# Performance work log

Measured on AMD Instinct MI355X. Metric: run time of the kernel, lower is better.

## Reference

```python
import jax, jax.numpy as jnp
import numpy as np

B, T, C = 1, 2048, 1024
H, D = 16, 64  # n_head, head_size (n_query_groups == n_head -> plain MHA)


def build_rope_cache(seq_len, n_elem, base=10000):
    theta = 1.0 / (base ** (jnp.arange(0, n_elem, 2, dtype=jnp.float32) / n_elem))
    idx_theta = jnp.outer(jnp.arange(seq_len, dtype=jnp.float32), theta)
    idx_theta = jnp.concatenate([idx_theta, idx_theta], axis=-1)  # torch .repeat(1, 2)
    return jnp.cos(idx_theta), jnp.sin(idx_theta)


def apply_rope(x, cos, sin):
    d = x.shape[-1]
    x1, x2 = x[..., : d // 2], x[..., d // 2 :]
    rotated = jnp.concatenate([-x2, x1], axis=-1)
    return x * cos + rotated * sin


def fastmax_attention(q, k, v):
    """Fastmax: first-order Taylor approx of softmax attention, causal, O(n*d^2).
    score(i,j) = 1 + q_i . k_j (temperature=1, zero RPE, no dropout);
    out_i = sum_{j<=i} score*v_j / sum_{j<=i} score, via causal cumulative sums."""
    n = q.shape[2]
    kcum = jnp.cumsum(k, axis=2)                                       # (B,H,T,D)
    kvcum = jnp.cumsum(jnp.einsum('bhnd,bhne->bhnde', k, v), axis=2)   # (B,H,T,D,D)
    den = jnp.arange(1, n + 1, dtype=q.dtype) + jnp.einsum('bhnd,bhnd->bhn', q, kcum)
    num = jnp.cumsum(v, axis=2) + jnp.einsum('bhnd,bhnde->bhne', q, kvcum)
    return num / den[..., None]


def setup_inputs() -> dict:
    key = jax.random.key(0)
    k1, k2, k3 = jax.random.split(key, 3)
    scale = 0.02
    x = jax.random.normal(k1, (B, T, C), dtype=jnp.float32)
    w_attn = jax.random.normal(k2, (3 * H * D, C), dtype=jnp.float32) * scale
    w_proj = jax.random.normal(k3, (C, H * D), dtype=jnp.float32) * scale
    cos, sin = build_rope_cache(T, D)
    return {"x": x, "w_attn": w_attn, "w_proj": w_proj, "cos": cos, "sin": sin}


def reference(x, w_attn, w_proj, cos, sin):
    Bx, Tx, Cx = x.shape
    qkv = x @ w_attn.T                                  # (B,T,3HD)
    qkv = qkv.reshape(Bx, Tx, H, 3, D).transpose(0, 2, 3, 1, 4)  # (B,H,3,T,D)
    q, k, v = qkv[:, :, 0], qkv[:, :, 1], qkv[:, :, 2]
    q = apply_rope(q, cos, sin)
    k = apply_rope(k, cos, sin)
    y = fastmax_attention(q, k, v)                      # (B,H,T,D)
    y = y.transpose(0, 2, 1, 3).reshape(Bx, Tx, H * D)
    return y @ w_proj.T
```

## Files before the change

### kernel.cpp

```cpp
#include <hip/hip_runtime.h>

#define T_LEN 2048
#define C_DIM 1024
#define H_NUM 16
#define D_DIM 64
#define QKV_N (3 * H_NUM * D_DIM)
#define L_CHK 64
#define NC (T_LEN / L_CHK)

typedef _Float16 h8 __attribute__((ext_vector_type(8)));
typedef _Float16 h4 __attribute__((ext_vector_type(4)));
typedef float f32x4 __attribute__((ext_vector_type(4)));

__global__ __launch_bounds__(256) void split3_f16(
    const float* __restrict__ x, _Float16* __restrict__ xh,
    _Float16* __restrict__ xl, const float* __restrict__ wa,
    _Float16* __restrict__ wah, _Float16* __restrict__ wal,
    const float* __restrict__ wp, _Float16* __restrict__ wph) {
  int i = (blockIdx.x * 256 + threadIdx.x) * 8;
  const float* src;
  _Float16 *dh, *dl = nullptr;
  int base;
  if (i < 2097152) {
    src = x; dh = xh; dl = xl; base = i;
  } else if (i < 2097152 + 3145728) {
    src = wa; dh = wah; dl = wal; base = i - 2097152;
  } else {
    src = wp; dh = wph; base = i - 5242880;
  }
  float4 a = *(const float4*)(src + base);
  float4 b = *(const float4*)(src + base + 4);
  float v[8] = {a.x, a.y, a.z, a.w, b.x, b.y, b.z, b.w};
  h8 hv, lv;
#pragma unroll
  for (int j = 0; j < 8; ++j) {
    float s = v[j] * 64.f;
    _Float16 h = (_Float16)s;
    hv[j] = h;
    lv[j] = (_Float16)(s - (float)h);
  }
  *(h8*)(dh + base) = hv;
  if (dl) *(h8*)(dl + base) = lv;
}

template <int BN, bool ROPE, bool SPLIT3>
__global__ __launch_bounds__(256) void gemm_nt_f16(
    const _Float16* __restrict__ Ah, const _Float16* __restrict__ Al,
    const _Float16* __restrict__ Bh, const _Float16* __restrict__ Bl,
    float* __restrict__ C, const float* __restrict__ cosb,
    const float* __restrict__ sinb, float* __restrict__ qout,
    float* __restrict__ kout, float* __restrict__ vout, int M, int N, int K,
    float outscale) {
  constexpr int NJ = BN / 32;
  constexpr int NARR = SPLIT3 ? 2 : 1;
  constexpr int GEMM_BYTES = (64 * 64 * 2 + BN * 64 * 2) * NARR;
  constexpr int ROPE_BYTES = ROPE ? (2 * 64 * 64 * 4) : 0;
  constexpr int SMEM_BYTES = GEMM_BYTES > ROPE_BYTES ? GEMM_BYTES : ROPE_BYTES;
  __shared__ __align__(16) char smem[SMEM_BYTES];
  _Float16* sAh = (_Float16*)smem;
  _Float16* sAl = sAh + 64 * 64;
  _Float16* sBh = sAh + 64 * 64 * NARR;
  _Float16* sBl = sBh + BN * 64;
  const int tid = threadIdx.x;
  const int wave = tid >> 6;
  const int lane = tid & 63;
  const int bm = blockIdx.y * 64;
  const int bn = blockIdx.x * BN;
  const int wm = wave >> 1;
  const int wn = wave & 1;
  const int srow = lane >> 3;
  const int sblk = ((lane & 7) ^ srow) * 8;
  const int quad = lane >> 4;
  const int lrow = lane & 15;

  f32x4 acc[2][NJ];
#pragma unroll
  for (int i = 0; i < 2; ++i)
#pragma unroll
    for (int j = 0; j < NJ; ++j) acc[i][j] = (f32x4){0.f, 0.f, 0.f, 0.f};

  for (int k0 = 0; k0 < K; k0 += 64) {
#pragma unroll
    for (int it = 0; it < 2; ++it) {
      const int ch = wave + it * 4;
      const int row = ch * 8 + srow;
      const _Float16* ga = Ah + (size_t)(bm + row) * K + k0 + sblk;
      __builtin_amdgcn_global_load_lds(
          (const __attribute__((address_space(1))) void*)ga,
          (__attribute__((address_space(3))) void*)(sAh + ch * 512), 16, 0, 0);
      if constexpr (SPLIT3) {
        const _Float16* gb = Al + (size_t)(bm + row) * K + k0 + sblk;
        __builtin_amdgcn_global_load_lds(
            (const __attribute__((address_space(1))) void*)gb,
            (__attribute__((address_space(3))) void*)(sAl + ch * 512), 16, 0,
            0);
      }
    }
#pragma unroll
    for (int it = 0; it < BN / 32; ++it) {
      const int ch = wave + it * 4;
      const int row = ch * 8 + srow;
      const _Float16* ga = Bh + (size_t)(bn + row) * K + k0 + sblk;
      __builtin_amdgcn_global_load_lds(
          (const __attribute__((address_space(1))) void*)ga,
          (__attribute__((address_space(3))) void*)(sBh + ch * 512), 16, 0, 0);
      if constexpr (SPLIT3) {
        const _Float16* gb = Bl + (size_t)(bn + row) * K + k0 + sblk;
        __builtin_amdgcn_global_load_lds(
            (const __attribute__((address_space(1))) void*)gb,
            (__attribute__((address_space(3))) void*)(sBl + ch * 512), 16, 0,
            0);
      }
    }
    __syncthreads();
#pragma unroll
    for (int kk = 0; kk < 2; ++kk) {
      h8 ah[2], al[2], bh[NJ], bl[NJ];
#pragma unroll
      for (int i = 0; i < 2; ++i) {
        const int row = wm * 32 + i * 16 + lrow;
        const int ra = row * 64 + (((kk * 4 + quad) ^ (row & 7)) * 8);
        ah[i] = *(const h8*)&sAh[ra];
        if constexpr (SPLIT3) al[i] = *(const h8*)&sAl[ra];
      }
#pragma unroll
      for (int j = 0; j < NJ; ++j) {
        const int row = wn * (BN / 2) + j * 16 + lrow;
        const int rb = row * 64 + (((kk * 4 + quad) ^ (row & 7)) * 8);
        bh[j] = *(const h8*)&sBh[rb];
        if constexpr (SPLIT3) bl[j] = *(const h8*)&sBl[rb];
      }
#pragma unroll
      for (int i = 0; i < 2; ++i)
#pragma unroll
        for (int j = 0; j < NJ; ++j) {
          acc[i][j] = __builtin_amdgcn_mfma_f32_16x16x32_f16(
              ah[i], bh[j], acc[i][j], 0, 0, 0);
          if constexpr (SPLIT3) {
            acc[i][j] = __builtin_amdgcn_mfma_f32_16x16x32_f16(
                ah[i], bl[j], acc[i][j], 0, 0, 0);
            acc[i][j] = __builtin_amdgcn_mfma_f32_16x16x32_f16(
                al[i], bh[j], acc[i][j], 0, 0, 0);
          }
        }
    }
    __syncthreads();
  }
  if constexpr (!ROPE) {
#pragma unroll
    for (int i = 0; i < 2; ++i) {
      const int rbase = bm + wm * 32 + i * 16 + quad * 4;
#pragma unroll
      for (int j = 0; j < NJ; ++j) {
        const int col = bn + wn * (BN / 2) + j * 16 + lrow;
#pragma unroll
        for (int r = 0; r < 4; ++r)
          C[(size_t)(rbase + r) * N + col] = acc[i][j][r] * outscale;
      }
    }
  } else {
    float* cs = (float*)smem;
    float* sn = cs + 4096;
#pragma unroll
    for (int m = 0; m < 4; ++m) {
      int el = (tid + m * 256) * 4;
      *(float4*)&cs[el] = *(const float4*)&cosb[bm * D_DIM + el];
      *(float4*)&sn[el] = *(const float4*)&sinb[bm * D_DIM + el];
    }
    __syncthreads();
    const int colbase = bn + wn * 64;
    const int type = (colbase >> 6) % 3;
    const int head = colbase / 192;
    float* dst = (type == 0) ? qout : (type == 1) ? kout : vout;
    const size_t hbase = (size_t)head * T_LEN * D_DIM;
#pragma unroll
    for (int i = 0; i < 2; ++i) {
      const int tloc0 = wm * 32 + i * 16 + quad * 4;
#pragma unroll
      for (int r = 0; r < 4; ++r) {
        const int tloc = tloc0 + r;
        float* trow = dst + hbase + (size_t)(bm + tloc) * D_DIM;
#pragma unroll
        for (int j = 0; j < NJ; ++j) {
          const int d = j * 16 + lrow;
          float val = acc[i][j][r] * outscale;
          if (type < 2) {
            float rotv = ((j < 2) ? -acc[i][j + 2][r] : acc[i][j - 2][r]) *
                         outscale;
            val = val * cs[tloc * D_DIM + d] + rotv * sn[tloc * D_DIM + d];
          }
          trow[d] = val;
        }
      }
    }
  }
}

__global__ __launch_bounds__(256) void chunk_kv(
    const float* __restrict__ k, const float* __restrict__ v,
    float* __restrict__ kvchunk, float* __restrict__ kschunk,
    float* __restrict__ vschunk) {
  __shared__ float Ks[L_CHK][D_DIM];
  __shared__ float Vs[L_CHK][D_DIM];
  int blk = blockIdx.x;
  const size_t off = ((size_t)(blk / NC) * T_LEN + (blk % NC) * L_CHK) * D_DIM;
  int tid = threadIdx.x;
#pragma unroll
  for (int m = 0; m < 4; ++m) {
    int el = (tid + m * 256) * 4;
    *(float4*)&((float*)Ks)[el] = *(const float4*)&k[off + el];
    *(float4*)&((float*)Vs)[el] = *(const float4*)&v[off + el];
  }
  __syncthreads();
  int e = tid & 63;
  int q2 = tid >> 6;
  float acc[16] = {};
  for (int t = 0; t < L_CHK; ++t) {
    float ve = Vs[t][e];
#pragma unroll
    for (int m = 0; m < 16; ++m) acc[m] += Ks[t][q2 * 16 + m] * ve;
  }
  float* outb = kvchunk + (size_t)blk * (D_DIM * D_DIM);
#pragma unroll
  for (int m = 0; m < 16; ++m) outb[(q2 * 16 + m) * D_DIM + e] = acc[m];
  if (tid < 64) {
    float s = 0.f;
    for (int t = 0; t < L_CHK; ++t) s += Ks[t][tid];
    kschunk[(size_t)blk * D_DIM + tid] = s;
  } else if (tid < 128) {
    float s = 0.f;
    for (int t = 0; t < L_CHK; ++t) s += Vs[t][tid - 64];
    vschunk[(size_t)blk * D_DIM + (tid - 64)] = s;
  }
}

__global__ __launch_bounds__(256) void scan_fused(
    const float* __restrict__ kvchunk, float* __restrict__ kvpref,
    const float* __restrict__ kschunk, const float* __restrict__ vschunk,
    float* __restrict__ kspref, float* __restrict__ vspref) {
  int b = blockIdx.x;
  int tid = threadIdx.x;
  if (b < 256) {
    int gid = b * 256 + tid;
    int h = gid >> 12;
    int de = gid & 4095;
    float vals[NC];
#pragma unroll
    for (int c = 0; c < NC; ++c)
      vals[c] = kvchunk[((size_t)(h * NC + c) << 12) + de];
    float run = 0.f;
#pragma unroll
    for (int c = 0; c < NC; ++c) {
      kvpref[((size_t)(h * NC + c) << 12) + de] = run;
      run += vals[c];
    }
  } else {
    int gid = (b - 256) * 256 + tid;
    int h = gid >> 6, d = gid & 63;
    float kv_[NC], vv_[NC];
#pragma unroll
    for (int c = 0; c < NC; ++c) {
      size_t idx = (size_t)(h * NC + c) * 64 + d;
      kv_[c] = kschunk[idx];
      vv_[c] = vschunk[idx];
    }
    float rk = 0.f, rv = 0.f;
#pragma unroll
    for (int c = 0; c < NC; ++c) {
      size_t idx = (size_t)(h * NC + c) * 64 + d;
      kspref[idx] = rk;
      vspref[idx] = rv;
      rk += kv_[c];
      rv += vv_[c];
    }
  }
}

__global__ __launch_bounds__(256) void attn_out(
    const float* __restrict__ q, const float* __restrict__ k,
    const float* __restrict__ v, const float* __restrict__ kvpref,
    const float* __restrict__ kspref, const float* __restrict__ vspref,
    _Float16* __restrict__ yh) {
  __shared__ float Ks[L_CHK * D_DIM];
  __shared__ float Vs[L_CHK * D_DIM];
  __shared__ float Ss[L_CHK][L_CHK + 1];
  int blk = blockIdx.x;
  int h = blk / NC, c = blk % NC;
  int tid = threadIdx.x;
  int r = tid & 63;
  int g = tid >> 6;
  const size_t off = ((size_t)h * T_LEN + c * L_CHK) * D_DIM;
#pragma unroll
  for (int m = 0; m < 4; ++m) {
    int el = (tid + m * 256) * 4;
    *(float4*)&Ks[el] = *(const float4*)&k[off + el];
    *(float4*)&Vs[el] = *(const float4*)&v[off + el];
  }
  float qv[D_DIM];
#pragma unroll
  for (int i = 0; i < 16; ++i) {
    float4 t4 = *(const float4*)&q[off + r * D_DIM + i * 4];
    qv[i * 4 + 0] = t4.x; qv[i * 4 + 1] = t4.y;
    qv[i * 4 + 2] = t4.z; qv[i * 4 + 3] = t4.w;
  }
  __syncthreads();
#pragma unroll
  for (int jj = 0; jj < 16; ++jj) {
    int j = g * 16 + jj;
    const float4* krow = (const float4*)&Ks[j * D_DIM];
    float sdot = 0.f;
#pragma unroll
    for (int i = 0; i < 16; ++i) {
      float4 kj = krow[i];
      sdot += qv[i * 4] * kj.x + qv[i * 4 + 1] * kj.y + qv[i * 4 + 2] * kj.z +
              qv[i * 4 + 3] * kj.w;
    }
    Ss[r][j] = (j <= r) ? (sdot + 1.f) : 0.f;
  }
  __syncthreads();
  const float* kvp = kvpref + (size_t)blk * (D_DIM * D_DIM);
#pragma unroll
  for (int m = 0; m < 4; ++m) {
    int el = (tid + m * 256) * 4;
    *(float4*)&Ks[el] = *(const float4*)&kvp[el];
  }
  __syncthreads();
  const float* ksp = kspref + (size_t)blk * D_DIM;
  const float* vsp = vspref + (size_t)blk * D_DIM;
  float den = (float)(c * L_CHK);
#pragma unroll
  for (int i = 0; i < 16; ++i) {
    float4 kk = *(const float4*)&ksp[i * 4];
    den += qv[i * 4] * kk.x + qv[i * 4 + 1] * kk.y + qv[i * 4 + 2] * kk.z +
           qv[i * 4 + 3] * kk.w;
  }
  float4 num[4];
#pragma unroll
  for (int i = 0; i < 4; ++i) num[i] = *(const float4*)&vsp[g * 16 + i * 4];
#pragma unroll
  for (int d = 0; d < D_DIM; ++d) {
    float qd = qv[d];
    const float4* kvrow = (const float4*)&Ks[d * D_DIM + g * 16];
#pragma unroll
    for (int i = 0; i < 4; ++i) {
      float4 k4 = kvrow[i];
      num[i].x += qd * k4.x; num[i].y += qd * k4.y;
      num[i].z += qd * k4.z; num[i].w += qd * k4.w;
    }
  }
  float rs = 0.f;
#pragma unroll 8
  for (int j = 0; j < L_CHK; ++j) {
    float f = Ss[r][j];
    rs += f;
    const float4* vrow = (const float4*)&Vs[j * D_DIM + g * 16];
#pragma unroll
    for (int i = 0; i < 4; ++i) {
      float4 v4 = vrow[i];
      num[i].x += f * v4.x; num[i].y += f * v4.y;
      num[i].z += f * v4.z; num[i].w += f * v4.w;
    }
  }
  den += rs;
  float inv = 1.f / den;
  int t = c * L_CHK + r;
  size_t ybase = (size_t)t * (H_NUM * D_DIM) + h * D_DIM + g * 16;
#pragma unroll
  for (int i = 0; i < 4; ++i) {
    h4 hv;
    hv[0] = (_Float16)(num[i].x * inv);
    hv[1] = (_Float16)(num[i].y * inv);
    hv[2] = (_Float16)(num[i].z * inv);
    hv[3] = (_Float16)(num[i].w * inv);
    *(h4*)&yh[ybase + i * 4] = hv;
  }
}

extern "C" void kernel_launch(void* const* d_in, const int* in_sizes, int n_in,
                              void* d_out, int out_size, void* d_ws,
                              size_t ws_size, hipStream_t stream) {
  const float* x = (const float*)d_in[0];
  const float* w_attn = (const float*)d_in[1];
  const float* w_proj = (const float*)d_in[2];
  const float* cosb = (const float*)d_in[3];
  const float* sinb = (const float*)d_in[4];
  float* out = (float*)d_out;

  char* ws = (char*)d_ws;
  float* kvchunk = (float*)ws;
  float* kvpref = (float*)(ws + 8388608);
  float* qbuf = (float*)(ws + 25165824);
  float* kbuf = (float*)(ws + 25165824 + 8388608);
  float* vbuf = (float*)(ws + 25165824 + 16777216);
  _Float16* xh = (_Float16*)(ws + 50331648);
  _Float16* xl = (_Float16*)(ws + 50331648 + 4194304);
  _Float16* yh = (_Float16*)(ws + 50331648);
  _Float16* wah = (_Float16*)(ws + 58720256);
  _Float16* wal = (_Float16*)(ws + 58720256 + 6291456);
  float* kschunk = (float*)(ws + 58720256);
  float* vschunk = (float*)(ws + 58720256 + 131072);
  float* kspref = (float*)(ws + 58720256 + 262144);
  float* vspref = (float*)(ws + 58720256 + 393216);
  _Float16* wph = (_Float16*)(ws + 71303168);

  split3_f16<<<3072, 256, 0, stream>>>(x, xh, xl, w_attn, wah, wal, w_proj,
                                       wph);

  {
    dim3 grid(QKV_N / 128, T_LEN / 64);
    gemm_nt_f16<128, true, true><<<grid, 256, 0, stream>>>(
        xh, xl, wah, wal, nullptr, cosb, sinb, qbuf, kbuf, vbuf, T_LEN, QKV_N,
        C_DIM, 1.f / 4096.f);
  }
  chunk_kv<<<H_NUM * NC, 256, 0, stream>>>(kbuf, vbuf, kvchunk, kschunk,
                                           vschunk);
  scan_fused<<<260, 256, 0, stream>>>(kvchunk, kvpref, kschunk, vschunk,
                                      kspref, vspref);
  attn_out<<<H_NUM * NC, 256, 0, stream>>>(qbuf, kbuf, vbuf, kvpref, kspref,
                                           vspref, yh);
  {
    dim3 grid(C_DIM / 64, T_LEN / 64);
    gemm_nt_f16<64, false, false><<<grid, 256, 0, stream>>>(
        yh, nullptr, wph, nullptr, out, nullptr, nullptr, nullptr, nullptr,
        nullptr, T_LEN, C_DIM, C_DIM, 1.f / 64.f);
  }
}
```

Before: 173.7 us.

## Move intra-chunk attention and chunk KV sums onto split-f16 MFMA

The QKV GEMM epilogue now writes q and k as hi/lo f16 pairs and also emits transposed k and v (via an LDS bounce) in hi/lo f16. The chunk KV outer-product kernel and the attention-output kernel are rewritten to use 16x16x32 f16 MFMA with three-term split products, including the score matrix, row sums and prefix-state contributions. This is meant to replace scalar FP32 FMA loops with matrix-core work and halve the bytes read per element. In exchange it adds extra epilogue writes and barriers in the GEMM and some precision loss from the split-f16 approximation.

```diff
diff --git a/kernel.cpp b/kernel.cpp
--- a/kernel.cpp
+++ b/kernel.cpp
@@ -43,18 +43,30 @@
   if (dl) *(h8*)(dl + base) = lv;
 }
 
+__device__ __forceinline__ void split8(float4 a, float4 b, h8& hi, h8& lo) {
+  float v[8] = {a.x, a.y, a.z, a.w, b.x, b.y, b.z, b.w};
+#pragma unroll
+  for (int m = 0; m < 8; ++m) {
+    _Float16 hh = (_Float16)v[m];
+    hi[m] = hh;
+    lo[m] = (_Float16)(v[m] - (float)hh);
+  }
+}
+
 template <int BN, bool ROPE, bool SPLIT3>
 __global__ __launch_bounds__(256) void gemm_nt_f16(
     const _Float16* __restrict__ Ah, const _Float16* __restrict__ Al,
     const _Float16* __restrict__ Bh, const _Float16* __restrict__ Bl,
     float* __restrict__ C, const float* __restrict__ cosb,
-    const float* __restrict__ sinb, float* __restrict__ qout,
-    float* __restrict__ kout, float* __restrict__ vout, int M, int N, int K,
-    float outscale) {
+    const float* __restrict__ sinb, _Float16* __restrict__ qh_,
+    _Float16* __restrict__ ql_, _Float16* __restrict__ kh_,
+    _Float16* __restrict__ kl_, _Float16* __restrict__ kTh_,
+    _Float16* __restrict__ kTl_, _Float16* __restrict__ vTh_,
+    _Float16* __restrict__ vTl_, int M, int N, int K, float outscale) {
   constexpr int NJ = BN / 32;
   constexpr int NARR = SPLIT3 ? 2 : 1;
   constexpr int GEMM_BYTES = (64 * 64 * 2 + BN * 64 * 2) * NARR;
-  constexpr int ROPE_BYTES = ROPE ? (2 * 64 * 64 * 4) : 0;
+  constexpr int ROPE_BYTES = ROPE ? (2 * 64 * 64 * 4 + 64 * 64 * 4) : 0;
   constexpr int SMEM_BYTES = GEMM_BYTES > ROPE_BYTES ? GEMM_BYTES : ROPE_BYTES;
   __shared__ __align__(16) char smem[SMEM_BYTES];
   _Float16* sAh = (_Float16*)smem;
@@ -161,6 +173,7 @@
   } else {
     float* cs = (float*)smem;
     float* sn = cs + 4096;
+    float* bounce = sn + 4096;
 #pragma unroll
     for (int m = 0; m < 4; ++m) {
       int el = (tid + m * 256) * 4;
@@ -171,66 +184,160 @@
     const int colbase = bn + wn * 64;
     const int type = (colbase >> 6) % 3;
     const int head = colbase / 192;
-    float* dst = (type == 0) ? qout : (type == 1) ? kout : vout;
-    const size_t hbase = (size_t)head * T_LEN * D_DIM;
-#pragma unroll
-    for (int i = 0; i < 2; ++i) {
-      const int tloc0 = wm * 32 + i * 16 + quad * 4;
+    const size_t hb = (size_t)head * T_LEN * D_DIM;
+    float fv[2][4][4];
+#pragma unroll
+    for (int i = 0; i < 2; ++i)
 #pragma unroll
       for (int r = 0; r < 4; ++r) {
-        const int tloc = tloc0 + r;
-        float* trow = dst + hbase + (size_t)(bm + tloc) * D_DIM;
-#pragma unroll
-        for (int j = 0; j < NJ; ++j) {
+        const int tloc = wm * 32 + i * 16 + quad * 4 + r;
+#pragma unroll
+        for (int j = 0; j < 4; ++j) {
           const int d = j * 16 + lrow;
           float val = acc[i][j][r] * outscale;
           if (type < 2) {
-            float rotv = ((j < 2) ? -acc[i][j + 2][r] : acc[i][j - 2][r]) *
-                         outscale;
+            float rotv =
+                ((j < 2) ? -acc[i][j + 2][r] : acc[i][j - 2][r]) * outscale;
             val = val * cs[tloc * D_DIM + d] + rotv * sn[tloc * D_DIM + d];
           }
-          trow[d] = val;
+          fv[i][r][j] = val;
         }
       }
-    }
-  }
-}
-
-__global__ __launch_bounds__(256) void chunk_kv(
-    const float* __restrict__ k, const float* __restrict__ v,
+    if (type < 2) {
+      _Float16* dh = (type == 0 ? qh_ : kh_) + hb;
+      _Float16* dl = (type == 0 ? ql_ : kl_) + hb;
+#pragma unroll
+      for (int i = 0; i < 2; ++i)
+#pragma unroll
+        for (int r = 0; r < 4; ++r) {
+          const size_t trow =
+              (size_t)(bm + wm * 32 + i * 16 + quad * 4 + r) * D_DIM;
+#pragma unroll
+          for (int j = 0; j < 4; ++j) {
+            const int d = j * 16 + lrow;
+            float f = fv[i][r][j];
+            _Float16 hh = (_Float16)f;
+            dh[trow + d] = hh;
+            dl[trow + d] = (_Float16)(f - (float)hh);
+          }
+        }
+    }
+    const bool doT = (type >= 1);
+    _Float16* th = (type == 1 ? kTh_ : vTh_) + hb;
+    _Float16* tl = (type == 1 ? kTl_ : vTl_) + hb;
+#pragma unroll
+    for (int half = 0; half < 2; ++half) {
+      __syncthreads();
+      if (wn == half && doT) {
+#pragma unroll
+        for (int i = 0; i < 2; ++i)
+#pragma unroll
+          for (int r = 0; r < 4; ++r) {
+            const int tloc = wm * 32 + i * 16 + quad * 4 + r;
+#pragma unroll
+            for (int j = 0; j < 4; ++j) {
+              const int d = j * 16 + lrow;
+              bounce[tloc * 64 + (d ^ tloc)] = fv[i][r][j];
+            }
+          }
+      }
+      __syncthreads();
+      if (wn == half && doT) {
+        const int lt = wm * 64 + lane;
+        const int e = lt >> 1;
+        const int tg0 = (lt & 1) * 32;
+#pragma unroll
+        for (int s8 = 0; s8 < 4; ++s8) {
+          h8 hv, lv;
+#pragma unroll
+          for (int s = 0; s < 8; ++s) {
+            const int t = tg0 + s8 * 8 + s;
+            float f = bounce[t * 64 + (e ^ t)];
+            _Float16 hh = (_Float16)f;
+            hv[s] = hh;
+            lv[s] = (_Float16)(f - (float)hh);
+          }
+          *(h8*)&th[(size_t)e * T_LEN + bm + tg0 + s8 * 8] = hv;
+          *(h8*)&tl[(size_t)e * T_LEN + bm + tg0 + s8 * 8] = lv;
+        }
+      }
+    }
+  }
+}
+
+__global__ __launch_bounds__(256) void chunk_kvT(
+    const _Float16* __restrict__ kTh, const _Float16* __restrict__ kTl,
+    const _Float16* __restrict__ vTh, const _Float16* __restrict__ vTl,
     float* __restrict__ kvchunk, float* __restrict__ kschunk,
     float* __restrict__ vschunk) {
-  __shared__ float Ks[L_CHK][D_DIM];
-  __shared__ float Vs[L_CHK][D_DIM];
-  int blk = blockIdx.x;
-  const size_t off = ((size_t)(blk / NC) * T_LEN + (blk % NC) * L_CHK) * D_DIM;
-  int tid = threadIdx.x;
-#pragma unroll
-  for (int m = 0; m < 4; ++m) {
-    int el = (tid + m * 256) * 4;
-    *(float4*)&((float*)Ks)[el] = *(const float4*)&k[off + el];
-    *(float4*)&((float*)Vs)[el] = *(const float4*)&v[off + el];
-  }
-  __syncthreads();
-  int e = tid & 63;
-  int q2 = tid >> 6;
-  float acc[16] = {};
-  for (int t = 0; t < L_CHK; ++t) {
-    float ve = Vs[t][e];
-#pragma unroll
-    for (int m = 0; m < 16; ++m) acc[m] += Ks[t][q2 * 16 + m] * ve;
-  }
-  float* outb = kvchunk + (size_t)blk * (D_DIM * D_DIM);
-#pragma unroll
-  for (int m = 0; m < 16; ++m) outb[(q2 * 16 + m) * D_DIM + e] = acc[m];
+  const int blk = blockIdx.x;
+  const int h = blk / NC, c = blk % NC;
+  const int tid = threadIdx.x;
+  const int wave = tid >> 6, lane = tid & 63;
+  const int quad = lane >> 4, lrow = lane & 15;
+  const size_t hb = (size_t)h * D_DIM * T_LEN;
+  const int tb = c * L_CHK;
+  h8 avh[2], avl[2];
+  {
+    const _Float16* pa = vTh + hb + (size_t)(wave * 16 + lrow) * T_LEN + tb +
+                         quad * 8;
+    const _Float16* pal = vTl + hb + (size_t)(wave * 16 + lrow) * T_LEN + tb +
+                          quad * 8;
+    avh[0] = *(const h8*)pa;
+    avh[1] = *(const h8*)(pa + 32);
+    avl[0] = *(const h8*)pal;
+    avl[1] = *(const h8*)(pal + 32);
+  }
+  f32x4 accv[4];
+#pragma unroll
+  for (int dt = 0; dt < 4; ++dt) accv[dt] = (f32x4){0.f, 0.f, 0.f, 0.f};
+#pragma unroll
+  for (int dt = 0; dt < 4; ++dt) {
+    const _Float16* pb = kTh + hb + (size_t)(dt * 16 + lrow) * T_LEN + tb +
+                         quad * 8;
+    const _Float16* pbl = kTl + hb + (size_t)(dt * 16 + lrow) * T_LEN + tb +
+                          quad * 8;
+#pragma unroll
+    for (int ks = 0; ks < 2; ++ks) {
+      h8 bh = *(const h8*)(pb + ks * 32);
+      h8 bl = *(const h8*)(pbl + ks * 32);
+      accv[dt] = __builtin_amdgcn_mfma_f32_16x16x32_f16(avh[ks], bh, accv[dt],
+                                                        0, 0, 0);
+      accv[dt] = __builtin_amdgcn_mfma_f32_16x16x32_f16(avh[ks], bl, accv[dt],
+                                                        0, 0, 0);
+      accv[dt] = __builtin_amdgcn_mfma_f32_16x16x32_f16(avl[ks], bh, accv[dt],
+                                                        0, 0, 0);
+    }
+  }
+  float* ob = kvchunk + (size_t)blk * (D_DIM * D_DIM);
+#pragma unroll
+  for (int dt = 0; dt < 4; ++dt)
+#pragma unroll
+    for (int r = 0; r < 4; ++r)
+      ob[(wave * 16 + quad * 4 + r) * D_DIM + dt * 16 + lrow] = accv[dt][r];
   if (tid < 64) {
+    const _Float16* p = kTh + hb + (size_t)tid * T_LEN + tb;
+    const _Float16* pl = kTl + hb + (size_t)tid * T_LEN + tb;
     float s = 0.f;
-    for (int t = 0; t < L_CHK; ++t) s += Ks[t][tid];
+#pragma unroll
+    for (int i = 0; i < 8; ++i) {
+      h8 a = *(const h8*)(p + i * 8), b = *(const h8*)(pl + i * 8);
+#pragma unroll
+      for (int m = 0; m < 8; ++m) s += (float)a[m] + (float)b[m];
+    }
     kschunk[(size_t)blk * D_DIM + tid] = s;
   } else if (tid < 128) {
+    const int e = tid - 64;
+    const _Float16* p = vTh + hb + (size_t)e * T_LEN + tb;
+    const _Float16* pl = vTl + hb + (size_t)e * T_LEN + tb;
     float s = 0.f;
-    for (int t = 0; t < L_CHK; ++t) s += Vs[t][tid - 64];
-    vschunk[(size_t)blk * D_DIM + (tid - 64)] = s;
+#pragma unroll
+    for (int i = 0; i < 8; ++i) {
+      h8 a = *(const h8*)(p + i * 8), b = *(const h8*)(pl + i * 8);
+#pragma unroll
+      for (int m = 0; m < 8; ++m) s += (float)a[m] + (float)b[m];
+    }
+    vschunk[(size_t)blk * D_DIM + e] = s;
   }
 }
 
@@ -276,103 +383,150 @@
   }
 }
 
-__global__ __launch_bounds__(256) void attn_out(
-    const float* __restrict__ q, const float* __restrict__ k,
-    const float* __restrict__ v, const float* __restrict__ kvpref,
-    const float* __restrict__ kspref, const float* __restrict__ vspref,
-    _Float16* __restrict__ yh) {
-  __shared__ float Ks[L_CHK * D_DIM];
-  __shared__ float Vs[L_CHK * D_DIM];
-  __shared__ float Ss[L_CHK][L_CHK + 1];
-  int blk = blockIdx.x;
-  int h = blk / NC, c = blk % NC;
-  int tid = threadIdx.x;
-  int r = tid & 63;
-  int g = tid >> 6;
-  const size_t off = ((size_t)h * T_LEN + c * L_CHK) * D_DIM;
-#pragma unroll
-  for (int m = 0; m < 4; ++m) {
-    int el = (tid + m * 256) * 4;
-    *(float4*)&Ks[el] = *(const float4*)&k[off + el];
-    *(float4*)&Vs[el] = *(const float4*)&v[off + el];
-  }
-  float qv[D_DIM];
-#pragma unroll
-  for (int i = 0; i < 16; ++i) {
-    float4 t4 = *(const float4*)&q[off + r * D_DIM + i * 4];
-    qv[i * 4 + 0] = t4.x; qv[i * 4 + 1] = t4.y;
-    qv[i * 4 + 2] = t4.z; qv[i * 4 + 3] = t4.w;
-  }
-  __syncthreads();
-#pragma unroll
-  for (int jj = 0; jj < 16; ++jj) {
-    int j = g * 16 + jj;
-    const float4* krow = (const float4*)&Ks[j * D_DIM];
-    float sdot = 0.f;
-#pragma unroll
-    for (int i = 0; i < 16; ++i) {
-      float4 kj = krow[i];
-      sdot += qv[i * 4] * kj.x + qv[i * 4 + 1] * kj.y + qv[i * 4 + 2] * kj.z +
-              qv[i * 4 + 3] * kj.w;
-    }
-    Ss[r][j] = (j <= r) ? (sdot + 1.f) : 0.f;
-  }
-  __syncthreads();
+__global__ __launch_bounds__(256) void attn_mfma(
+    const _Float16* __restrict__ qh, const _Float16* __restrict__ ql,
+    const _Float16* __restrict__ kh, const _Float16* __restrict__ kl,
+    const _Float16* __restrict__ vTh, const _Float16* __restrict__ vTl,
+    const float* __restrict__ kvpref, const float* __restrict__ kspref,
+    const float* __restrict__ vspref, _Float16* __restrict__ yh) {
+  __shared__ __align__(16) _Float16 sS[2][4][16 * 64];
+  const int blk = blockIdx.x;
+  const int h = blk / NC, c = blk % NC;
+  const int tid = threadIdx.x;
+  const int wave = tid >> 6, lane = tid & 63;
+  const int quad = lane >> 4, lrow = lane & 15;
+  const size_t hb = (size_t)h * T_LEN * D_DIM;
+  const size_t hbT = (size_t)h * D_DIM * T_LEN;
+  const int t0 = c * L_CHK;
+  const f32x4 z4 = {0.f, 0.f, 0.f, 0.f};
+  h8 aqh[2], aql[2];
+  {
+    const _Float16* pq =
+        qh + hb + (size_t)(t0 + wave * 16 + lrow) * D_DIM + quad * 8;
+    const _Float16* pql =
+        ql + hb + (size_t)(t0 + wave * 16 + lrow) * D_DIM + quad * 8;
+    aqh[0] = *(const h8*)pq;
+    aqh[1] = *(const h8*)(pq + 32);
+    aql[0] = *(const h8*)pql;
+    aql[1] = *(const h8*)(pql + 32);
+  }
+  f32x4 sacc[4];
+#pragma unroll
+  for (int jt = 0; jt < 4; ++jt) sacc[jt] = z4;
+#pragma unroll
+  for (int jt = 0; jt < 4; ++jt) {
+    const _Float16* pk =
+        kh + hb + (size_t)(t0 + jt * 16 + lrow) * D_DIM + quad * 8;
+    const _Float16* pkl =
+        kl + hb + (size_t)(t0 + jt * 16 + lrow) * D_DIM + quad * 8;
+#pragma unroll
+    for (int ks = 0; ks < 2; ++ks) {
+      h8 bh = *(const h8*)(pk + ks * 32);
+      h8 bl = *(const h8*)(pkl + ks * 32);
+      sacc[jt] = __builtin_amdgcn_mfma_f32_16x16x32_f16(aqh[ks], bh, sacc[jt],
+                                                        0, 0, 0);
+      sacc[jt] = __builtin_amdgcn_mfma_f32_16x16x32_f16(aqh[ks], bl, sacc[jt],
+                                                        0, 0, 0);
+      sacc[jt] = __builtin_amdgcn_mfma_f32_16x16x32_f16(aql[ks], bh, sacc[jt],
+                                                        0, 0, 0);
+    }
+  }
+  _Float16* shp = &sS[0][wave][0];
+  _Float16* slp = &sS[1][wave][0];
+#pragma unroll
+  for (int jt = 0; jt < 4; ++jt)
+#pragma unroll
+    for (int r = 0; r < 4; ++r) {
+      const int row = quad * 4 + r;
+      const int j = jt * 16 + lrow;
+      const int rglob = wave * 16 + row;
+      float s = (j <= rglob) ? (sacc[jt][r] + 1.f) : 0.f;
+      _Float16 hh = (_Float16)s;
+      const int adr = row * 64 + ((((j >> 3) ^ (row & 7)) << 3) | (j & 7));
+      shp[adr] = hh;
+      slp[adr] = (_Float16)(s - (float)hh);
+    }
+  h8 ash[2], asl[2];
+#pragma unroll
+  for (int ks = 0; ks < 2; ++ks) {
+    const int adr = lrow * 64 + (((ks * 4 + quad) ^ (lrow & 7)) << 3);
+    ash[ks] = *(const h8*)&shp[adr];
+    asl[ks] = *(const h8*)&slp[adr];
+  }
+  h8 ones;
+#pragma unroll
+  for (int m = 0; m < 8; ++m) ones[m] = (_Float16)1.0f;
+  f32x4 rs = z4;
+#pragma unroll
+  for (int ks = 0; ks < 2; ++ks) {
+    rs = __builtin_amdgcn_mfma_f32_16x16x32_f16(ash[ks], ones, rs, 0, 0, 0);
+    rs = __builtin_amdgcn_mfma_f32_16x16x32_f16(asl[ks], ones, rs, 0, 0, 0);
+  }
+  f32x4 oacc[4];
+#pragma unroll
+  for (int et = 0; et < 4; ++et) oacc[et] = z4;
+#pragma unroll
+  for (int et = 0; et < 4; ++et) {
+    const _Float16* pv =
+        vTh + hbT + (size_t)(et * 16 + lrow) * T_LEN + t0 + quad * 8;
+    const _Float16* pvl =
+        vTl + hbT + (size_t)(et * 16 + lrow) * T_LEN + t0 + quad * 8;
+#pragma unroll
+    for (int ks = 0; ks < 2; ++ks) {
+      h8 bh = *(const h8*)(pv + ks * 32);
+      h8 bl = *(const h8*)(pvl + ks * 32);
+      oacc[et] = __builtin_amdgcn_mfma_f32_16x16x32_f16(ash[ks], bh, oacc[et],
+                                                        0, 0, 0);
+      oacc[et] = __builtin_amdgcn_mfma_f32_16x16x32_f16(ash[ks], bl, oacc[et],
+                                                        0, 0, 0);
+      oacc[et] = __builtin_amdgcn_mfma_f32_16x16x32_f16(asl[ks], bh, oacc[et],
+                                                        0, 0, 0);
+    }
+  }
   const float* kvp = kvpref + (size_t)blk * (D_DIM * D_DIM);
 #pragma unroll
-  for (int m = 0; m < 4; ++m) {
-    int el = (tid + m * 256) * 4;
-    *(float4*)&Ks[el] = *(const float4*)&kvp[el];
-  }
-  __syncthreads();
+  for (int et = 0; et < 4; ++et) {
+#pragma unroll
+    for (int ks = 0; ks < 2; ++ks) {
+      const float* pb = kvp + (et * 16 + lrow) * D_DIM + ks * 32 + quad * 8;
+      float4 b0 = *(const float4*)pb;
+      float4 b1 = *(const float4*)(pb + 4);
+      h8 bh, bl;
+      split8(b0, b1, bh, bl);
+      oacc[et] = __builtin_amdgcn_mfma_f32_16x16x32_f16(aqh[ks], bh, oacc[et],
+                                                        0, 0, 0);
+      oacc[et] = __builtin_amdgcn_mfma_f32_16x16x32_f16(aqh[ks], bl, oacc[et],
+                                                        0, 0, 0);
+      oacc[et] = __builtin_amdgcn_mfma_f32_16x16x32_f16(aql[ks], bh, oacc[et],
+                                                        0, 0, 0);
+    }
+  }
   const float* ksp = kspref + (size_t)blk * D_DIM;
+  f32x4 kacc = z4;
+#pragma unroll
+  for (int ks = 0; ks < 2; ++ks) {
+    const float* pb = ksp + ks * 32 + quad * 8;
+    float4 b0 = *(const float4*)pb;
+    float4 b1 = *(const float4*)(pb + 4);
+    h8 bh, bl;
+    split8(b0, b1, bh, bl);
+    kacc = __builtin_amdgcn_mfma_f32_16x16x32_f16(aqh[ks], bh, kacc, 0, 0, 0);
+    kacc = __builtin_amdgcn_mfma_f32_16x16x32_f16(aqh[ks], bl, kacc, 0, 0, 0);
+    kacc = __builtin_amdgcn_mfma_f32_16x16x32_f16(aql[ks], bh, kacc, 0, 0, 0);
+  }
   const float* vsp = vspref + (size_t)blk * D_DIM;
-  float den = (float)(c * L_CHK);
-#pragma unroll
-  for (int i = 0; i < 16; ++i) {
-    float4 kk = *(const float4*)&ksp[i * 4];
-    den += qv[i * 4] * kk.x + qv[i * 4 + 1] * kk.y + qv[i * 4 + 2] * kk.z +
-           qv[i * 4 + 3] * kk.w;
-  }
-  float4 num[4];
-#pragma unroll
-  for (int i = 0; i < 4; ++i) num[i] = *(const float4*)&vsp[g * 16 + i * 4];
-#pragma unroll
-  for (int d = 0; d < D_DIM; ++d) {
-    float qd = qv[d];
-    const float4* kvrow = (const float4*)&Ks[d * D_DIM + g * 16];
-#pragma unroll
-    for (int i = 0; i < 4; ++i) {
-      float4 k4 = kvrow[i];
-      num[i].x += qd * k4.x; num[i].y += qd * k4.y;
-      num[i].z += qd * k4.z; num[i].w += qd * k4.w;
-    }
-  }
-  float rs = 0.f;
-#pragma unroll 8
-  for (int j = 0; j < L_CHK; ++j) {
-    float f = Ss[r][j];
-    rs += f;
-    const float4* vrow = (const float4*)&Vs[j * D_DIM + g * 16];
-#pragma unroll
-    for (int i = 0; i < 4; ++i) {
-      float4 v4 = vrow[i];
-      num[i].x += f * v4.x; num[i].y += f * v4.y;
-      num[i].z += f * v4.z; num[i].w += f * v4.w;
-    }
-  }
-  den += rs;
-  float inv = 1.f / den;
-  int t = c * L_CHK + r;
-  size_t ybase = (size_t)t * (H_NUM * D_DIM) + h * D_DIM + g * 16;
-#pragma unroll
-  for (int i = 0; i < 4; ++i) {
-    h4 hv;
-    hv[0] = (_Float16)(num[i].x * inv);
-    hv[1] = (_Float16)(num[i].y * inv);
-    hv[2] = (_Float16)(num[i].z * inv);
-    hv[3] = (_Float16)(num[i].w * inv);
-    *(h4*)&yh[ybase + i * 4] = hv;
+#pragma unroll
+  for (int r = 0; r < 4; ++r) {
+    const int row = wave * 16 + quad * 4 + r;
+    const float den = (float)(c * L_CHK) + rs[r] + kacc[r];
+    const float inv = 1.f / den;
+    const size_t ybase = (size_t)(t0 + row) * (H_NUM * D_DIM) + h * D_DIM;
+#pragma unroll
+    for (int et = 0; et < 4; ++et) {
+      const int e = et * 16 + lrow;
+      const float num = oacc[et][r] + vsp[e];
+      yh[ybase + e] = (_Float16)(num * inv);
+    }
   }
 }
 
@@ -387,21 +541,27 @@
   float* out = (float*)d_out;
 
   char* ws = (char*)d_ws;
+  const size_t MB = 1048576;
   float* kvchunk = (float*)ws;
-  float* kvpref = (float*)(ws + 8388608);
-  float* qbuf = (float*)(ws + 25165824);
-  float* kbuf = (float*)(ws + 25165824 + 8388608);
-  float* vbuf = (float*)(ws + 25165824 + 16777216);
-  _Float16* xh = (_Float16*)(ws + 50331648);
-  _Float16* xl = (_Float16*)(ws + 50331648 + 4194304);
-  _Float16* yh = (_Float16*)(ws + 50331648);
-  _Float16* wah = (_Float16*)(ws + 58720256);
-  _Float16* wal = (_Float16*)(ws + 58720256 + 6291456);
-  float* kschunk = (float*)(ws + 58720256);
-  float* vschunk = (float*)(ws + 58720256 + 131072);
-  float* kspref = (float*)(ws + 58720256 + 262144);
-  float* vspref = (float*)(ws + 58720256 + 393216);
-  _Float16* wph = (_Float16*)(ws + 71303168);
+  float* kvpref = (float*)(ws + 8 * MB);
+  _Float16* qh = (_Float16*)(ws + 16 * MB);
+  _Float16* ql = (_Float16*)(ws + 20 * MB);
+  _Float16* kh = (_Float16*)(ws + 24 * MB);
+  _Float16* kl = (_Float16*)(ws + 28 * MB);
+  _Float16* kTh = (_Float16*)(ws + 32 * MB);
+  _Float16* kTl = (_Float16*)(ws + 36 * MB);
+  _Float16* vTh = (_Float16*)(ws + 40 * MB);
+  _Float16* vTl = (_Float16*)(ws + 44 * MB);
+  _Float16* xh = (_Float16*)(ws + 48 * MB);
+  _Float16* xl = (_Float16*)(ws + 52 * MB);
+  _Float16* yh = (_Float16*)(ws + 48 * MB);
+  _Float16* wah = (_Float16*)(ws + 56 * MB);
+  _Float16* wal = (_Float16*)(ws + 62 * MB);
+  float* kschunk = (float*)(ws + 56 * MB);
+  float* vschunk = (float*)(ws + 56 * MB + 131072);
+  float* kspref = (float*)(ws + 56 * MB + 262144);
+  float* vspref = (float*)(ws + 56 * MB + 393216);
+  _Float16* wph = (_Float16*)(ws + 68 * MB);
 
   split3_f16<<<3072, 256, 0, stream>>>(x, xh, xl, w_attn, wah, wal, w_proj,
                                        wph);
@@ -409,19 +569,20 @@
   {
     dim3 grid(QKV_N / 128, T_LEN / 64);
     gemm_nt_f16<128, true, true><<<grid, 256, 0, stream>>>(
-        xh, xl, wah, wal, nullptr, cosb, sinb, qbuf, kbuf, vbuf, T_LEN, QKV_N,
-        C_DIM, 1.f / 4096.f);
-  }
-  chunk_kv<<<H_NUM * NC, 256, 0, stream>>>(kbuf, vbuf, kvchunk, kschunk,
-                                           vschunk);
+        xh, xl, wah, wal, nullptr, cosb, sinb, qh, ql, kh, kl, kTh, kTl, vTh,
+        vTl, T_LEN, QKV_N, C_DIM, 1.f / 4096.f);
+  }
+  chunk_kvT<<<H_NUM * NC, 256, 0, stream>>>(kTh, kTl, vTh, vTl, kvchunk,
+                                            kschunk, vschunk);
   scan_fused<<<260, 256, 0, stream>>>(kvchunk, kvpref, kschunk, vschunk,
                                       kspref, vspref);
-  attn_out<<<H_NUM * NC, 256, 0, stream>>>(qbuf, kbuf, vbuf, kvpref, kspref,
-                                           vspref, yh);
+  attn_mfma<<<H_NUM * NC, 256, 0, stream>>>(qh, ql, kh, kl, vTh, vTl, kvpref,
+                                            kspref, vspref, yh);
   {
     dim3 grid(C_DIM / 64, T_LEN / 64);
     gemm_nt_f16<64, false, false><<<grid, 256, 0, stream>>>(
         yh, nullptr, wph, nullptr, out, nullptr, nullptr, nullptr, nullptr,
-        nullptr, T_LEN, C_DIM, C_DIM, 1.f / 64.f);
-  }
-}
+        nullptr, nullptr, nullptr, nullptr, nullptr, nullptr, T_LEN, C_DIM,
+        C_DIM, 1.f / 64.f);
+  }
+}
```

Result: no change. 171.3 us (-1.4%).
